# Kernel optimization log

Hardware: AMD Instinct MI355X
Metric: run time of the kernel (lower is better)

The kernel has to match this reference:

```python
import jax, jax.numpy as jnp
import numpy as np

N = 4096   # nodes per side
B = 32     # graphs per batch
E = 65536  # edges per side
D = 128    # hidden dim
L = 4      # layers
H = 4      # heads


def setup_inputs() -> dict:
    key = jax.random.key(0)
    ks = jax.random.split(key, 20)
    s = 1.0 / np.sqrt(D)
    inp = {
        'x_s': jax.random.normal(ks[0], (N, D), jnp.float32),
        'x_t': jax.random.normal(ks[1], (N, D), jnp.float32),
        'edge_index_s': jax.random.randint(ks[2], (2, E), 0, N),
        'edge_attr_s': jax.random.uniform(ks[3], (E, D), jnp.float32),
        'edge_index_t': jax.random.randint(ks[4], (2, E), 0, N),
        'edge_attr_t': jax.random.uniform(ks[5], (E, D), jnp.float32),
        'batch_s': jnp.repeat(jnp.arange(B), N // B),
        'batch_t': jnp.repeat(jnp.arange(B), N // B),
        # stacked per-layer parameters (torch Linear layout: [out, in])
        'gnn_rel_w': jax.random.normal(ks[6], (L, D, D), jnp.float32) * s,
        'gnn_rel_b': jnp.zeros((L, D), jnp.float32),
        'gnn_root_w': jax.random.normal(ks[7], (L, D, D), jnp.float32) * s,
        'attn_in_w': jax.random.normal(ks[8], (L, 3 * D, D), jnp.float32) * s,
        'attn_in_b': jnp.zeros((L, 3 * D), jnp.float32),
        'attn_out_w': jax.random.normal(ks[9], (L, D, D), jnp.float32) * s,
        'attn_out_b': jnp.zeros((L, D), jnp.float32),
        'ln_g': jnp.ones((L, D), jnp.float32),
        'ln_b': jnp.zeros((L, D), jnp.float32),
        'gate_w': jax.random.normal(ks[10], (D, 1), jnp.float32) * s,
        'gate_b': jnp.zeros((1,), jnp.float32),
    }
    return inp


def _graph_conv(x, src, dst, ew, w_rel, b_rel, w_root):
    # message = edge_weight * x_j, aggr='mean' over target nodes
    msg = ew * x[src]                                   # [E, D]
    agg = jax.ops.segment_sum(msg, dst, num_segments=N)
    cnt = jax.ops.segment_sum(jnp.ones((msg.shape[0], 1), x.dtype), dst, num_segments=N)
    mean = agg / jnp.maximum(cnt, 1.0)
    return mean @ w_rel.T + b_rel + x @ w_root.T


def _mha(qx, kx, w_in, b_in, w_out, b_out, mask):
    dh = D // H
    q = (qx @ w_in[:D].T + b_in[:D]).reshape(-1, H, dh)
    k = (kx @ w_in[D:2 * D].T + b_in[D:2 * D]).reshape(-1, H, dh)
    v = (kx @ w_in[2 * D:].T + b_in[2 * D:]).reshape(-1, H, dh)
    scores = jnp.einsum('qhd,khd->hqk', q, k) * (1.0 / np.sqrt(dh))
    scores = jnp.where(mask[None], -jnp.inf, scores)
    a = jax.nn.softmax(scores, axis=-1)
    o = jnp.einsum('hqk,khd->qhd', a, v).reshape(-1, D)
    return o @ w_out.T + b_out


def _layernorm(x, g, b, eps=1e-5):
    mu = jnp.mean(x, axis=-1, keepdims=True)
    var = jnp.mean((x - mu) ** 2, axis=-1, keepdims=True)
    return (x - mu) * jax.lax.rsqrt(var + eps) * g + b


def _pool(x, batch, gw, gb):
    # GlobalAttention: gate = sigmoid(Linear(x)); softmax per graph; weighted sum
    gate = jax.nn.sigmoid(x @ gw + gb)                  # [N, 1]
    m = jax.ops.segment_max(gate, batch, num_segments=B)
    e = jnp.exp(gate - m[batch])
    z = jax.ops.segment_sum(e, batch, num_segments=B)
    alpha = e / z[batch]
    return jax.ops.segment_sum(alpha * x, batch, num_segments=B)  # [B, D]


def reference(x_s, x_t, edge_index_s, edge_attr_s, edge_index_t, edge_attr_t,
              batch_s, batch_t, gnn_rel_w, gnn_rel_b, gnn_root_w,
              attn_in_w, attn_in_b, attn_out_w, attn_out_b, ln_g, ln_b,
              gate_w, gate_b):
    src_s, dst_s = edge_index_s[0], edge_index_s[1]
    src_t, dst_t = edge_index_t[0], edge_index_t[1]
    mask = batch_s[:, None] != batch_t[None, :]         # True = blocked
    for i in range(L):
        x_s = _graph_conv(x_s, src_s, dst_s, edge_attr_s, gnn_rel_w[i], gnn_rel_b[i], gnn_root_w[i])
        x_t = _graph_conv(x_t, src_t, dst_t, edge_attr_t, gnn_rel_w[i], gnn_rel_b[i], gnn_root_w[i])
        o_s = _mha(x_s, x_t, attn_in_w[i], attn_in_b[i], attn_out_w[i], attn_out_b[i], mask)
        o_t = _mha(x_t, x_s, attn_in_w[i], attn_in_b[i], attn_out_w[i], attn_out_b[i], mask.T)
        x_s = _layernorm(o_s, ln_g[i], ln_b[i])
        x_t = _layernorm(o_t, ln_g[i], ln_b[i])
    p_s = _pool(x_s, batch_s, gate_w, gate_b)
    p_t = _pool(x_t, batch_t, gate_w, gate_b)
    p_s = p_s / jnp.maximum(jnp.linalg.norm(p_s, axis=-1, keepdims=True), 1e-12)
    p_t = p_t / jnp.maximum(jnp.linalg.norm(p_t, axis=-1, keepdims=True), 1e-12)
    return jnp.sum(p_s * p_t, axis=-1)                  # [B]
```

## Files before the change

kernel.cpp:

```cpp
#include <hip/hip_runtime.h>
#include <math.h>

#define N_NODES 4096
#define NROWS   8192
#define BGRAPH  32
#define NEDGE   65536
#define DIM     128
#define NLAYER  4
#define NHEAD   4
#define DHEAD   32
#define QDIM    384

typedef _Float16 half8v __attribute__((ext_vector_type(8)));
typedef _Float16 half4v __attribute__((ext_vector_type(4)));
typedef _Float16 half2v __attribute__((ext_vector_type(2)));
typedef float f32x4 __attribute__((ext_vector_type(4)));

__device__ inline f32x4 MFMA(half8v a, half8v b, f32x4 c) {
    return __builtin_amdgcn_mfma_f32_16x16x32_f16(a, b, c, 0, 0, 0);
}

__device__ inline void cvt4(const float* __restrict__ s, _Float16* __restrict__ d, int i) {
    float4 v = ((const float4*)s)[i];
    half4v h;
    h[0] = (_Float16)v.x; h[1] = (_Float16)v.y;
    h[2] = (_Float16)v.z; h[3] = (_Float16)v.w;
    *(half4v*)(d + (size_t)i * 4) = h;
}

__global__ __launch_bounds__(256) void cvth_kernel(
    const float* __restrict__ x_s, const float* __restrict__ x_t,
    const float* __restrict__ out_w,
    const int* __restrict__ dst_s, const int* __restrict__ dst_t,
    _Float16* __restrict__ x16, _Float16* __restrict__ outw16,
    int* __restrict__ cnt)
{
    int gid = blockIdx.x * 256 + threadIdx.x, gs = gridDim.x * 256;
    const int nx = N_NODES * DIM / 4;
    const int nw = NLAYER * DIM * DIM / 4;
    for (int i = gid; i < nx; i += gs) cvt4(x_s, x16, i);
    for (int i = gid; i < nx; i += gs) cvt4(x_t, x16 + N_NODES * DIM, i);
    for (int i = gid; i < nw; i += gs) cvt4(out_w, outw16, i);
    for (int i = gid; i < 2 * NEDGE; i += gs) {
        int side = i >> 16, e = i & (NEDGE - 1);
        const int* dd = side ? dst_t : dst_s;
        atomicAdd(&cnt[side * N_NODES + dd[e]], 1);
    }
}

__global__ __launch_bounds__(256) void scan_kernel(
    const int* __restrict__ cnt, int* __restrict__ row_start, int* __restrict__ cursor)
{
    int side = blockIdx.x;
    int t = threadIdx.x;
    __shared__ int part[256];
    int local[16];
    int s = 0;
    #pragma unroll
    for (int j = 0; j < 16; ++j) { local[j] = cnt[side * N_NODES + t * 16 + j]; s += local[j]; }
    part[t] = s;
    __syncthreads();
    for (int off = 1; off < 256; off <<= 1) {
        int v = (t >= off) ? part[t - off] : 0;
        __syncthreads();
        part[t] += v;
        __syncthreads();
    }
    int run = (t == 0) ? 0 : part[t - 1];
    #pragma unroll
    for (int j = 0; j < 16; ++j) {
        int idx = t * 16 + j;
        row_start[side * (N_NODES + 1) + idx] = run;
        cursor[side * N_NODES + idx] = run;
        run += local[j];
    }
    if (t == 255) row_start[side * (N_NODES + 1) + N_NODES] = run;
}

__global__ __launch_bounds__(256) void rg_kernel(
    const int* __restrict__ src_s, const int* __restrict__ dst_s,
    const int* __restrict__ src_t, const int* __restrict__ dst_t,
    const float* __restrict__ ea_s, const float* __restrict__ ea_t,
    int* __restrict__ cursor, int* __restrict__ srcs, _Float16* __restrict__ ea16s)
{
    int t = threadIdx.x;
    int g16 = t >> 4, sub = t & 15, lane = t & 63;
    int ef = blockIdx.x * 16 + g16;
    int side = ef >> 16, e = ef & (NEDGE - 1);
    const int* dd = side ? dst_t : dst_s;
    const int* ss = side ? src_t : src_s;
    const float* ea = side ? ea_t : ea_s;
    int pos = 0;
    if (sub == 0) pos = atomicAdd(&cursor[side * N_NODES + dd[e]], 1);
    pos = __shfl(pos, lane & ~15);
    if (sub == 0) srcs[side * NEDGE + pos] = ss[e];
    const float* sp = ea + (size_t)e * DIM + sub * 8;
    float4 v0 = *(const float4*)(sp);
    float4 v1 = *(const float4*)(sp + 4);
    half8v h;
    h[0]=(_Float16)v0.x; h[1]=(_Float16)v0.y; h[2]=(_Float16)v0.z; h[3]=(_Float16)v0.w;
    h[4]=(_Float16)v1.x; h[5]=(_Float16)v1.y; h[6]=(_Float16)v1.z; h[7]=(_Float16)v1.w;
    *(half8v*)(ea16s + (size_t)(side * NEDGE + pos) * DIM + sub * 8) = h;
}

__global__ __launch_bounds__(256) void wprod_kernel(
    const float* __restrict__ in_w, const float* __restrict__ root_w,
    const float* __restrict__ rel_w, const float* __restrict__ rel_b,
    const float* __restrict__ in_b,
    _Float16* __restrict__ wq16, float* __restrict__ beff)
{
    int gid = blockIdx.x * 256 + threadIdx.x;
    const int MT = NLAYER * 2 * QDIM * DIM;
    if (gid < MT) {
        int L = gid / (2 * QDIM * DIM);
        int r = gid % (2 * QDIM * DIM);
        int m = r / (QDIM * DIM);
        int r2 = r % (QDIM * DIM);
        int i = r2 / DIM, k = r2 % DIM;
        const float* Win = in_w + (size_t)L * QDIM * DIM;
        const float* B = (m ? rel_w : root_w) + (size_t)L * DIM * DIM;
        float s = 0.f;
        #pragma unroll 4
        for (int j = 0; j < DIM; ++j) s += Win[i * DIM + j] * B[j * DIM + k];
        wq16[gid] = (_Float16)s;
    } else {
        int r = gid - MT;
        if (r >= NLAYER * QDIM) return;
        int L = r / QDIM, i = r % QDIM;
        const float* Win = in_w + (size_t)L * QDIM * DIM;
        const float* br = rel_b + (size_t)L * DIM;
        float s = in_b[(size_t)L * QDIM + i];
        #pragma unroll 4
        for (int j = 0; j < DIM; ++j) s += Win[i * DIM + j] * br[j];
        beff[r] = s;
    }
}

__global__ __launch_bounds__(64) void agg_kernel(
    const int* __restrict__ srcs, const _Float16* __restrict__ ea16s,
    const int* __restrict__ row_start,
    const _Float16* __restrict__ x16, _Float16* __restrict__ agg16)
{
    int n = blockIdx.x, side = blockIdx.y;
    int lane = threadIdx.x;
    const int* sp = srcs + side * NEDGE;
    const _Float16* ep = ea16s + (size_t)side * NEDGE * DIM + lane * 2;
    const _Float16* xp = x16 + (size_t)side * N_NODES * DIM + lane * 2;
    int rs = row_start[side * (N_NODES + 1) + n];
    int re = row_start[side * (N_NODES + 1) + n + 1];
    float ax = 0.f, ay = 0.f;
    int i = rs;
    for (; i + 2 <= re; i += 2) {
        int s0 = sp[i], s1 = sp[i + 1];
        half2v w0 = *(const half2v*)(ep + (size_t)i * DIM);
        half2v w1 = *(const half2v*)(ep + (size_t)(i + 1) * DIM);
        half2v x0 = *(const half2v*)(xp + (size_t)s0 * DIM);
        half2v x1 = *(const half2v*)(xp + (size_t)s1 * DIM);
        ax += (float)w0[0] * (float)x0[0] + (float)w1[0] * (float)x1[0];
        ay += (float)w0[1] * (float)x0[1] + (float)w1[1] * (float)x1[1];
    }
    if (i < re) {
        int s0 = sp[i];
        half2v w0 = *(const half2v*)(ep + (size_t)i * DIM);
        half2v x0 = *(const half2v*)(xp + (size_t)s0 * DIM);
        ax += (float)w0[0] * (float)x0[0];
        ay += (float)w0[1] * (float)x0[1];
    }
    float sc = 1.0f / (float)max(re - rs, 1);
    half2v o; o[0] = (_Float16)(ax * sc); o[1] = (_Float16)(ay * sc);
    *(half2v*)(agg16 + (size_t)(side * N_NODES + n) * DIM + lane * 2) = o;
}

__global__ __launch_bounds__(256) void qkv2_mfma(
    const _Float16* __restrict__ x16, const _Float16* __restrict__ agg16,
    const _Float16* __restrict__ wq,
    const float* __restrict__ beff,
    _Float16* __restrict__ qb16)
{
    int tid = threadIdx.x;
    int wave = tid >> 6, lane = tid & 63;
    int wm = wave >> 1, wn = wave & 1;
    int row0 = blockIdx.x * 64 + wm * 32;
    int col0 = blockIdx.y * 64 + wn * 32;
    int lr = lane & 15;
    int lk = (lane >> 4) * 8;
    f32x4 zero = {0.f, 0.f, 0.f, 0.f};
    f32x4 acc[2][2] = {{zero, zero}, {zero, zero}};
    #pragma unroll
    for (int s = 0; s < 2; ++s) {
        const _Float16* A = s ? agg16 : x16;
        const _Float16* W = wq + (size_t)s * QDIM * DIM;
        const _Float16* Ap0 = A + (size_t)(row0 + lr) * DIM + lk;
        const _Float16* Ap1 = A + (size_t)(row0 + 16 + lr) * DIM + lk;
        const _Float16* Wp0 = W + (size_t)(col0 + lr) * DIM + lk;
        const _Float16* Wp1 = W + (size_t)(col0 + 16 + lr) * DIM + lk;
        #pragma unroll
        for (int k0 = 0; k0 < DIM; k0 += 32) {
            half8v a0 = *(const half8v*)(Ap0 + k0);
            half8v a1 = *(const half8v*)(Ap1 + k0);
            half8v b0 = *(const half8v*)(Wp0 + k0);
            half8v b1 = *(const half8v*)(Wp1 + k0);
            acc[0][0] = MFMA(a0, b0, acc[0][0]);
            acc[0][1] = MFMA(a0, b1, acc[0][1]);
            acc[1][0] = MFMA(a1, b0, acc[1][0]);
            acc[1][1] = MFMA(a1, b1, acc[1][1]);
        }
    }
    int g4 = (lane >> 4) * 4;
    #pragma unroll
    for (int fc = 0; fc < 2; ++fc) {
        int col = col0 + fc * 16 + lr;
        float bv = beff[col];
        #pragma unroll
        for (int fr = 0; fr < 2; ++fr) {
            int rbase = row0 + fr * 16 + g4;
            #pragma unroll
            for (int j = 0; j < 4; ++j) {
                float v = acc[fr][fc][j] + bv;
                qb16[(size_t)(rbase + j) * QDIM + col] = (_Float16)v;
            }
        }
    }
}

__global__ __launch_bounds__(256) void attn_mfma_kernel(
    const _Float16* __restrict__ qkv, _Float16* __restrict__ o16)
{
    int g = blockIdx.x, dir = blockIdx.y;
    int h = blockIdx.z >> 1, rh = blockIdx.z & 1;
    int qoff  = dir ? N_NODES : 0;
    int kvoff = dir ? 0 : N_NODES;
    int t = threadIdx.x;
    int w = t >> 6, lane = t & 63;
    int lr = lane & 15, g4 = lane >> 4;
    __shared__ _Float16 VT[32][136];
    __shared__ _Float16 P[4][16][136];
    {
        int kk = t >> 1, dd = (t & 1) * 16;
        const _Float16* vp = qkv + (size_t)(kvoff + g * 128 + kk) * QDIM + 2 * DIM + h * DHEAD + dd;
        half8v v0 = *(const half8v*)(vp);
        half8v v1 = *(const half8v*)(vp + 8);
        #pragma unroll
        for (int j = 0; j < 8; ++j) { VT[dd + j][kk] = v0[j]; VT[dd + 8 + j][kk] = v1[j]; }
    }
    int qrow0 = qoff + g * 128 + rh * 64 + w * 16;
    const _Float16* qp = qkv + (size_t)(qrow0 + lr) * QDIM + h * DHEAD + g4 * 8;
    half8v qfrag = *(const half8v*)qp;
    f32x4 zero = {0.f, 0.f, 0.f, 0.f};
    f32x4 S[8];
    #pragma unroll
    for (int kf = 0; kf < 8; ++kf) {
        const _Float16* kp = qkv + (size_t)(kvoff + g * 128 + kf * 16 + lr) * QDIM
                             + DIM + h * DHEAD + g4 * 8;
        S[kf] = MFMA(qfrag, *(const half8v*)kp, zero);
    }
    const float scale = 0.17677669529663687f;
    #pragma unroll
    for (int j = 0; j < 4; ++j) {
        float m = -INFINITY;
        #pragma unroll
        for (int kf = 0; kf < 8; ++kf) m = fmaxf(m, S[kf][j]);
        m *= scale;
        #pragma unroll
        for (int mk = 1; mk < 16; mk <<= 1) m = fmaxf(m, __shfl_xor(m, mk));
        float pj[8];
        float l = 0.f;
        #pragma unroll
        for (int kf = 0; kf < 8; ++kf) {
            float pv = __expf(S[kf][j] * scale - m);
            pj[kf] = pv; l += pv;
        }
        #pragma unroll
        for (int mk = 1; mk < 16; mk <<= 1) l += __shfl_xor(l, mk);
        float linv = 1.0f / l;
        int row = g4 * 4 + j;
        #pragma unroll
        for (int kf = 0; kf < 8; ++kf)
            P[w][row][kf * 16 + lr] = (_Float16)(pj[kf] * linv);
    }
    __syncthreads();
    f32x4 O[2] = {zero, zero};
    #pragma unroll
    for (int ks = 0; ks < 4; ++ks) {
        half8v pa = *(const half8v*)&P[w][lr][ks * 32 + g4 * 8];
        #pragma unroll
        for (int df = 0; df < 2; ++df) {
            half8v vb = *(const half8v*)&VT[df * 16 + lr][ks * 32 + g4 * 8];
            O[df] = MFMA(pa, vb, O[df]);
        }
    }
    #pragma unroll
    for (int df = 0; df < 2; ++df)
        #pragma unroll
        for (int j = 0; j < 4; ++j)
            o16[(size_t)(qrow0 + g4 * 4 + j) * DIM + h * DHEAD + df * 16 + lr] =
                (_Float16)O[df][j];
}

__global__ __launch_bounds__(256) void gemm_ln_mfma(
    const _Float16* __restrict__ A, const _Float16* __restrict__ W,
    const float* __restrict__ bias, const float* __restrict__ gamma,
    const float* __restrict__ beta, _Float16* __restrict__ outh)
{
    int tid = threadIdx.x;
    int wave = tid >> 6, lane = tid & 63;
    int row0 = blockIdx.x * 16;
    int col0 = wave * 32;
    int lr = lane & 15;
    int lk = (lane >> 4) * 8;
    f32x4 zero = {0.f, 0.f, 0.f, 0.f};
    f32x4 acc[2] = {zero, zero};
    const _Float16* Ap0 = A + (size_t)(row0 + lr) * DIM + lk;
    const _Float16* Wp0 = W + (size_t)(col0 + lr) * DIM + lk;
    const _Float16* Wp1 = W + (size_t)(col0 + 16 + lr) * DIM + lk;
    #pragma unroll
    for (int k0 = 0; k0 < DIM; k0 += 32) {
        half8v a0 = *(const half8v*)(Ap0 + k0);
        half8v b0 = *(const half8v*)(Wp0 + k0);
        half8v b1 = *(const half8v*)(Wp1 + k0);
        acc[0] = MFMA(a0, b0, acc[0]);
        acc[1] = MFMA(a0, b1, acc[1]);
    }
    int g = lane >> 4;
    float v[2][4];
    #pragma unroll
    for (int fc = 0; fc < 2; ++fc) {
        float bv = bias[col0 + fc * 16 + lr];
        #pragma unroll
        for (int j = 0; j < 4; ++j)
            v[fc][j] = acc[fc][j] + bv;
    }
    __shared__ float red_s[16][5];
    __shared__ float red_q[16][5];
    #pragma unroll
    for (int j = 0; j < 4; ++j) {
        float ss = v[0][j] + v[1][j];
        float qq = v[0][j] * v[0][j] + v[1][j] * v[1][j];
        #pragma unroll
        for (int m = 1; m < 16; m <<= 1) {
            ss += __shfl_xor(ss, m);
            qq += __shfl_xor(qq, m);
        }
        if (lr == 0) {
            red_s[g * 4 + j][wave] = ss;
            red_q[g * 4 + j][wave] = qq;
        }
    }
    __syncthreads();
    #pragma unroll
    for (int j = 0; j < 4; ++j) {
        int r = g * 4 + j;
        float S = red_s[r][0] + red_s[r][1] + red_s[r][2] + red_s[r][3];
        float Q = red_q[r][0] + red_q[r][1] + red_q[r][2] + red_q[r][3];
        float mu = S * (1.0f / 128.0f);
        float inv = rsqrtf(Q * (1.0f / 128.0f) - mu * mu + 1e-5f);
        #pragma unroll
        for (int fc = 0; fc < 2; ++fc) {
            int col = col0 + fc * 16 + lr;
            float o = (v[fc][j] - mu) * inv * gamma[col] + beta[col];
            outh[(size_t)(row0 + r) * DIM + col] = (_Float16)o;
        }
    }
}

__global__ __launch_bounds__(256) void poolcos_kernel(
    const _Float16* __restrict__ x16, const float* __restrict__ gw,
    const float* __restrict__ gb, float* __restrict__ out)
{
    int g = blockIdx.x, t = threadIdx.x;
    int side = t >> 7, r = t & 127;
    __shared__ float sm[2][128];
    __shared__ float al[2][128];
    __shared__ float pl[2][DIM];
    const _Float16* xr = x16 + (size_t)(side * N_NODES + g * 128 + r) * DIM;
    float dot = gb[0];
    #pragma unroll
    for (int d = 0; d < DIM; d += 8) {
        half8v xv = *(const half8v*)(xr + d);
        #pragma unroll
        for (int u = 0; u < 8; ++u) dot += (float)xv[u] * gw[d + u];
    }
    float gate = 1.0f / (1.0f + __expf(-dot));
    sm[side][r] = gate; __syncthreads();
    for (int sN = 64; sN > 0; sN >>= 1) {
        if (r < sN) sm[side][r] = fmaxf(sm[side][r], sm[side][r + sN]);
        __syncthreads();
    }
    float m = sm[side][0]; __syncthreads();
    float e = __expf(gate - m);
    sm[side][r] = e; __syncthreads();
    for (int sN = 64; sN > 0; sN >>= 1) {
        if (r < sN) sm[side][r] += sm[side][r + sN];
        __syncthreads();
    }
    al[side][r] = e / sm[side][0];
    __syncthreads();
    int d = t & 127;
    float acc = 0.0f;
    const _Float16* xg = x16 + (size_t)(side * N_NODES + g * 128) * DIM;
    for (int n = 0; n < 128; ++n) acc += al[side][n] * (float)xg[(size_t)n * DIM + d];
    pl[side][d] = acc;
    __syncthreads();
    if (t < 64) {
        float a0 = pl[0][t], a1 = pl[0][64 + t];
        float b0 = pl[1][t], b1 = pl[1][64 + t];
        float saa = a0 * a0 + a1 * a1;
        float sbb = b0 * b0 + b1 * b1;
        float sab = a0 * b0 + a1 * b1;
        #pragma unroll
        for (int off = 32; off; off >>= 1) {
            saa += __shfl_down(saa, off);
            sbb += __shfl_down(sbb, off);
            sab += __shfl_down(sab, off);
        }
        if (t == 0) {
            float na = fmaxf(sqrtf(saa), 1e-12f);
            float nb = fmaxf(sqrtf(sbb), 1e-12f);
            out[g] = sab / (na * nb);
        }
    }
}

extern "C" void kernel_launch(void* const* d_in, const int* in_sizes, int n_in,
                              void* d_out, int out_size, void* d_ws, size_t ws_size,
                              hipStream_t stream)
{
    const float* x_s    = (const float*)d_in[0];
    const float* x_t    = (const float*)d_in[1];
    const int*   ei_s   = (const int*)d_in[2];
    const float* ea_s   = (const float*)d_in[3];
    const int*   ei_t   = (const int*)d_in[4];
    const float* ea_t   = (const float*)d_in[5];
    const float* rel_w  = (const float*)d_in[8];
    const float* rel_b  = (const float*)d_in[9];
    const float* root_w = (const float*)d_in[10];
    const float* in_w   = (const float*)d_in[11];
    const float* in_b   = (const float*)d_in[12];
    const float* out_w  = (const float*)d_in[13];
    const float* out_b  = (const float*)d_in[14];
    const float* g_ln   = (const float*)d_in[15];
    const float* b_ln   = (const float*)d_in[16];
    const float* gate_w = (const float*)d_in[17];
    const float* gate_b = (const float*)d_in[18];
    float* out = (float*)d_out;

    const size_t RD = (size_t)NROWS * DIM;
    _Float16* h16p = (_Float16*)d_ws;
    _Float16* x16    = h16p; h16p += RD;
    _Float16* agg16  = h16p; h16p += RD;
    _Float16* qb16   = h16p; h16p += RD * 3;
    _Float16* o16    = h16p; h16p += RD;
    _Float16* ea16s  = h16p; h16p += (size_t)2 * NEDGE * DIM;
    _Float16* outw16 = h16p; h16p += (size_t)NLAYER * DIM * DIM;
    _Float16* wq16   = h16p; h16p += (size_t)NLAYER * 2 * QDIM * DIM;
    float* fws = (float*)h16p;
    float* beff = fws; fws += NLAYER * QDIM;
    int* iws = (int*)fws;
    int* cnt       = iws; iws += 2 * N_NODES;
    int* cursor    = iws; iws += 2 * N_NODES;
    int* row_start = iws; iws += 2 * (N_NODES + 1);
    int* srcs      = iws; iws += 2 * NEDGE;

    const int* src_s = ei_s, *dst_s = ei_s + NEDGE;
    const int* src_t = ei_t, *dst_t = ei_t + NEDGE;

    hipMemsetAsync(cnt, 0, 2 * N_NODES * 4, stream);
    cvth_kernel<<<512, 256, 0, stream>>>(x_s, x_t, out_w, dst_s, dst_t,
                                         x16, outw16, cnt);
    scan_kernel<<<2, 256, 0, stream>>>(cnt, row_start, cursor);
    rg_kernel<<<2 * NEDGE / 16, 256, 0, stream>>>(src_s, dst_s, src_t, dst_t,
                                                  ea_s, ea_t, cursor, srcs, ea16s);
    wprod_kernel<<<(NLAYER * 2 * QDIM * DIM + NLAYER * QDIM + 255) / 256, 256, 0, stream>>>(
        in_w, root_w, rel_w, rel_b, in_b, wq16, beff);

    dim3 gq(NROWS / 64, QDIM / 64);
    dim3 gagg(N_NODES, 2);
    dim3 gattn(BGRAPH, 2, NHEAD * 2);

    for (int i = 0; i < NLAYER; ++i) {
        const _Float16* wq   = wq16   + (size_t)i * 2 * QDIM * DIM;
        const float*    be   = beff   + (size_t)i * QDIM;
        const _Float16* wout = outw16 + (size_t)i * DIM * DIM;
        const float*    bout = out_b  + (size_t)i * DIM;
        const float*    lg   = g_ln   + (size_t)i * DIM;
        const float*    lb   = b_ln   + (size_t)i * DIM;

        agg_kernel<<<gagg, 64, 0, stream>>>(srcs, ea16s, row_start, x16, agg16);
        qkv2_mfma<<<gq, 256, 0, stream>>>(x16, agg16, wq, be, qb16);
        attn_mfma_kernel<<<gattn, 256, 0, stream>>>(qb16, o16);
        gemm_ln_mfma<<<NROWS / 16, 256, 0, stream>>>(o16, wout, bout, lg, lb, x16);
    }

    poolcos_kernel<<<BGRAPH, 256, 0, stream>>>(x16, gate_w, gate_b, out);
}
```

Before: 220.9 us.

## Fuse attention with output projection and LayerNorm into one kernel

Merges the per-head attention kernel and the out-projection+LayerNorm GEMM into a single kernel. Each block now handles 16 query rows across all 4 heads (one wave per head), stages the attention output in shared memory, then runs the out-projection MFMA and LayerNorm in place. This removes one launch per layer and the o16 round trip through global memory. In exchange, each block redundantly loads the full V for all heads and K per wave. Parallelism also changes: the grid is now 512 blocks of 16 rows instead of 512 blocks of 64 rows per head.

```diff
diff --git a/kernel.cpp b/kernel.cpp
--- a/kernel.cpp
+++ b/kernel.cpp
@@ -223,35 +223,43 @@
     }
 }
 
-__global__ __launch_bounds__(256) void attn_mfma_kernel(
-    const _Float16* __restrict__ qkv, _Float16* __restrict__ o16)
-{
-    int g = blockIdx.x, dir = blockIdx.y;
-    int h = blockIdx.z >> 1, rh = blockIdx.z & 1;
+__global__ __launch_bounds__(256) void attn_oln_kernel(
+    const _Float16* __restrict__ qkv, const _Float16* __restrict__ outw,
+    const float* __restrict__ bias, const float* __restrict__ gamma,
+    const float* __restrict__ beta, _Float16* __restrict__ x16out)
+{
+    int g = blockIdx.x, dir = blockIdx.y, rb = blockIdx.z;
     int qoff  = dir ? N_NODES : 0;
     int kvoff = dir ? 0 : N_NODES;
     int t = threadIdx.x;
     int w = t >> 6, lane = t & 63;
     int lr = lane & 15, g4 = lane >> 4;
-    __shared__ _Float16 VT[32][136];
-    __shared__ _Float16 P[4][16][136];
-    {
-        int kk = t >> 1, dd = (t & 1) * 16;
-        const _Float16* vp = qkv + (size_t)(kvoff + g * 128 + kk) * QDIM + 2 * DIM + h * DHEAD + dd;
+    __shared__ _Float16 VT[NHEAD][32][136];
+    __shared__ _Float16 P[NHEAD][16][136];
+    __shared__ float red_s[16][5], red_q[16][5];
+    f32x4 zero = {0.f, 0.f, 0.f, 0.f};
+    for (int kk = lane; kk < 128; kk += 64) {
+        const _Float16* vp = qkv + (size_t)(kvoff + g * 128 + kk) * QDIM + 2 * DIM + w * DHEAD;
         half8v v0 = *(const half8v*)(vp);
         half8v v1 = *(const half8v*)(vp + 8);
-        #pragma unroll
-        for (int j = 0; j < 8; ++j) { VT[dd + j][kk] = v0[j]; VT[dd + 8 + j][kk] = v1[j]; }
-    }
-    int qrow0 = qoff + g * 128 + rh * 64 + w * 16;
-    const _Float16* qp = qkv + (size_t)(qrow0 + lr) * QDIM + h * DHEAD + g4 * 8;
+        half8v v2 = *(const half8v*)(vp + 16);
+        half8v v3 = *(const half8v*)(vp + 24);
+        #pragma unroll
+        for (int j = 0; j < 8; ++j) {
+            VT[w][j][kk]      = v0[j];
+            VT[w][8 + j][kk]  = v1[j];
+            VT[w][16 + j][kk] = v2[j];
+            VT[w][24 + j][kk] = v3[j];
+        }
+    }
+    int qrow0 = qoff + g * 128 + rb * 16;
+    const _Float16* qp = qkv + (size_t)(qrow0 + lr) * QDIM + w * DHEAD + g4 * 8;
     half8v qfrag = *(const half8v*)qp;
-    f32x4 zero = {0.f, 0.f, 0.f, 0.f};
     f32x4 S[8];
     #pragma unroll
     for (int kf = 0; kf < 8; ++kf) {
         const _Float16* kp = qkv + (size_t)(kvoff + g * 128 + kf * 16 + lr) * QDIM
-                             + DIM + h * DHEAD + g4 * 8;
+                             + DIM + w * DHEAD + g4 * 8;
         S[kf] = MFMA(qfrag, *(const half8v*)kp, zero);
     }
     const float scale = 0.17677669529663687f;
@@ -278,87 +286,68 @@
         for (int kf = 0; kf < 8; ++kf)
             P[w][row][kf * 16 + lr] = (_Float16)(pj[kf] * linv);
     }
-    __syncthreads();
     f32x4 O[2] = {zero, zero};
     #pragma unroll
     for (int ks = 0; ks < 4; ++ks) {
         half8v pa = *(const half8v*)&P[w][lr][ks * 32 + g4 * 8];
         #pragma unroll
         for (int df = 0; df < 2; ++df) {
-            half8v vb = *(const half8v*)&VT[df * 16 + lr][ks * 32 + g4 * 8];
+            half8v vb = *(const half8v*)&VT[w][df * 16 + lr][ks * 32 + g4 * 8];
             O[df] = MFMA(pa, vb, O[df]);
         }
     }
+    __syncthreads();
+    _Float16 (*OL)[136] = P[0];
     #pragma unroll
     for (int df = 0; df < 2; ++df)
         #pragma unroll
         for (int j = 0; j < 4; ++j)
-            o16[(size_t)(qrow0 + g4 * 4 + j) * DIM + h * DHEAD + df * 16 + lr] =
-                (_Float16)O[df][j];
-}
-
-__global__ __launch_bounds__(256) void gemm_ln_mfma(
-    const _Float16* __restrict__ A, const _Float16* __restrict__ W,
-    const float* __restrict__ bias, const float* __restrict__ gamma,
-    const float* __restrict__ beta, _Float16* __restrict__ outh)
-{
-    int tid = threadIdx.x;
-    int wave = tid >> 6, lane = tid & 63;
-    int row0 = blockIdx.x * 16;
-    int col0 = wave * 32;
-    int lr = lane & 15;
-    int lk = (lane >> 4) * 8;
-    f32x4 zero = {0.f, 0.f, 0.f, 0.f};
-    f32x4 acc[2] = {zero, zero};
-    const _Float16* Ap0 = A + (size_t)(row0 + lr) * DIM + lk;
-    const _Float16* Wp0 = W + (size_t)(col0 + lr) * DIM + lk;
-    const _Float16* Wp1 = W + (size_t)(col0 + 16 + lr) * DIM + lk;
-    #pragma unroll
-    for (int k0 = 0; k0 < DIM; k0 += 32) {
-        half8v a0 = *(const half8v*)(Ap0 + k0);
-        half8v b0 = *(const half8v*)(Wp0 + k0);
-        half8v b1 = *(const half8v*)(Wp1 + k0);
-        acc[0] = MFMA(a0, b0, acc[0]);
-        acc[1] = MFMA(a0, b1, acc[1]);
-    }
-    int g = lane >> 4;
+            OL[g4 * 4 + j][w * DHEAD + df * 16 + lr] = (_Float16)O[df][j];
+    __syncthreads();
+    f32x4 acc2[2] = {zero, zero};
+    #pragma unroll
+    for (int kk = 0; kk < 4; ++kk) {
+        half8v a = *(const half8v*)&OL[lr][kk * 32 + g4 * 8];
+        #pragma unroll
+        for (int ct = 0; ct < 2; ++ct) {
+            const _Float16* wp = outw + (size_t)(w * 32 + ct * 16 + lr) * DIM + kk * 32 + g4 * 8;
+            acc2[ct] = MFMA(a, *(const half8v*)wp, acc2[ct]);
+        }
+    }
     float v[2][4];
     #pragma unroll
-    for (int fc = 0; fc < 2; ++fc) {
-        float bv = bias[col0 + fc * 16 + lr];
-        #pragma unroll
-        for (int j = 0; j < 4; ++j)
-            v[fc][j] = acc[fc][j] + bv;
-    }
-    __shared__ float red_s[16][5];
-    __shared__ float red_q[16][5];
+    for (int ct = 0; ct < 2; ++ct) {
+        float bv = bias[w * 32 + ct * 16 + lr];
+        #pragma unroll
+        for (int j = 0; j < 4; ++j) v[ct][j] = acc2[ct][j] + bv;
+    }
     #pragma unroll
     for (int j = 0; j < 4; ++j) {
         float ss = v[0][j] + v[1][j];
         float qq = v[0][j] * v[0][j] + v[1][j] * v[1][j];
         #pragma unroll
-        for (int m = 1; m < 16; m <<= 1) {
-            ss += __shfl_xor(ss, m);
-            qq += __shfl_xor(qq, m);
+        for (int mk = 1; mk < 16; mk <<= 1) {
+            ss += __shfl_xor(ss, mk);
+            qq += __shfl_xor(qq, mk);
         }
         if (lr == 0) {
-            red_s[g * 4 + j][wave] = ss;
-            red_q[g * 4 + j][wave] = qq;
+            red_s[g4 * 4 + j][w] = ss;
+            red_q[g4 * 4 + j][w] = qq;
         }
     }
     __syncthreads();
     #pragma unroll
     for (int j = 0; j < 4; ++j) {
-        int r = g * 4 + j;
-        float S = red_s[r][0] + red_s[r][1] + red_s[r][2] + red_s[r][3];
-        float Q = red_q[r][0] + red_q[r][1] + red_q[r][2] + red_q[r][3];
-        float mu = S * (1.0f / 128.0f);
-        float inv = rsqrtf(Q * (1.0f / 128.0f) - mu * mu + 1e-5f);
-        #pragma unroll
-        for (int fc = 0; fc < 2; ++fc) {
-            int col = col0 + fc * 16 + lr;
-            float o = (v[fc][j] - mu) * inv * gamma[col] + beta[col];
-            outh[(size_t)(row0 + r) * DIM + col] = (_Float16)o;
+        int row = g4 * 4 + j;
+        float Sv = red_s[row][0] + red_s[row][1] + red_s[row][2] + red_s[row][3];
+        float Qv = red_q[row][0] + red_q[row][1] + red_q[row][2] + red_q[row][3];
+        float mu = Sv * (1.0f / 128.0f);
+        float inv = rsqrtf(Qv * (1.0f / 128.0f) - mu * mu + 1e-5f);
+        #pragma unroll
+        for (int ct = 0; ct < 2; ++ct) {
+            int col = w * 32 + ct * 16 + lr;
+            float o = (v[ct][j] - mu) * inv * gamma[col] + beta[col];
+            x16out[(size_t)(qrow0 + row) * DIM + col] = (_Float16)o;
         }
     }
 }
@@ -449,7 +438,6 @@
     _Float16* x16    = h16p; h16p += RD;
     _Float16* agg16  = h16p; h16p += RD;
     _Float16* qb16   = h16p; h16p += RD * 3;
-    _Float16* o16    = h16p; h16p += RD;
     _Float16* ea16s  = h16p; h16p += (size_t)2 * NEDGE * DIM;
     _Float16* outw16 = h16p; h16p += (size_t)NLAYER * DIM * DIM;
     _Float16* wq16   = h16p; h16p += (size_t)NLAYER * 2 * QDIM * DIM;
@@ -475,7 +463,7 @@
 
     dim3 gq(NROWS / 64, QDIM / 64);
     dim3 gagg(N_NODES, 2);
-    dim3 gattn(BGRAPH, 2, NHEAD * 2);
+    dim3 gattn(BGRAPH, 2, 8);
 
     for (int i = 0; i < NLAYER; ++i) {
         const _Float16* wq   = wq16   + (size_t)i * 2 * QDIM * DIM;
@@ -487,8 +475,7 @@
 
         agg_kernel<<<gagg, 64, 0, stream>>>(srcs, ea16s, row_start, x16, agg16);
         qkv2_mfma<<<gq, 256, 0, stream>>>(x16, agg16, wq, be, qb16);
-        attn_mfma_kernel<<<gattn, 256, 0, stream>>>(qb16, o16);
-        gemm_ln_mfma<<<NROWS / 16, 256, 0, stream>>>(o16, wout, bout, lg, lb, x16);
+        attn_oln_kernel<<<gattn, 256, 0, stream>>>(qb16, wout, bout, lg, lb, x16);
     }
 
     poolcos_kernel<<<BGRAPH, 256, 0, stream>>>(x16, gate_w, gate_b, out);
```

Result: faster. 213.0 us (-3.6%).
